# Optimization experiments

Measured on AMD Instinct MI355X. Metric: run time of the kernel, lower is better.

The kernel has to match this reference:

```python
import jax, jax.numpy as jnp
import numpy as np

K = 16
D = 1024
B = 65536

# Row-major off-diagonal index order matching the torch double loop (i, j, i != j)
_ii, _jj = np.nonzero(~np.eye(K, dtype=bool))  # each (K*(K-1),), row-major
OFF_I = jnp.asarray(_ii)
OFF_J = jnp.asarray(_jj)
DIAG = jnp.arange(K)


def setup_inputs() -> dict:
    key = jax.random.key(0)
    k1, k2, k3, k4, k5 = jax.random.split(key, 5)
    scale_d = 1.0 / np.sqrt(D)
    return {
        "x": jax.random.normal(k1, (B, D), dtype=jnp.float32),
        "Wd": jax.random.normal(k2, (K, D), dtype=jnp.float32) * scale_d,
        "bd": jax.random.normal(k3, (K,), dtype=jnp.float32) * 0.1,
        "Wo": jax.random.normal(k4, (K * (K - 1), D), dtype=jnp.float32) * scale_d,
        "bo": jax.random.normal(k5, (K * (K - 1),), dtype=jnp.float32) * 0.1 - 3.0,
    }


def reference(x, Wd, bd, Wo, bo):
    # Diagonal gates: (B, K)
    c_diag = jax.nn.sigmoid(jnp.einsum("bd,kd->bk", x, Wd) + bd)
    # Off-diagonal values: (B, K*(K-1)), non-positive
    off_vals = -jax.nn.softplus(jnp.einsum("bd,kd->bk", x, Wo) + bo)
    C = jnp.zeros((x.shape[0], K, K), dtype=x.dtype)
    C = C.at[:, OFF_I, OFF_J].set(off_vals)
    C = C.at[:, DIAG, DIAG].set(c_diag)
    return C
```

## Files before the change

### kernel.cpp

```cpp
#include <hip/hip_runtime.h>
#include <hip/hip_bf16.h>
#include <stdint.h>


typedef __bf16 bf16x8 __attribute__((ext_vector_type(8)));
typedef float f32x4 __attribute__((ext_vector_type(4)));

#define THREADS 512
#define BM 128
#define KSTEPS 16
#define WTILE 32768
#define WBYTES (WTILE * KSTEPS)

__device__ __forceinline__ unsigned bf_rtne(unsigned u) {
  return (u + 0x7fffu + ((u >> 16) & 1u)) >> 16;
}
__device__ __forceinline__ unsigned pack2(float lo, float hi) {
  return bf_rtne(__float_as_uint(lo)) | (bf_rtne(__float_as_uint(hi)) << 16);
}

__device__ __forceinline__ void gload_lds16(const void* g, void* l) {
  __builtin_amdgcn_global_load_lds(
      (const __attribute__((address_space(1))) unsigned int*)g,
      (__attribute__((address_space(3))) unsigned int*)l, 16, 0, 0);
}

__global__ void prep_kernel(const float* __restrict__ Wd, const float* __restrict__ bd,
                            const float* __restrict__ Wo, const float* __restrict__ bo,
                            char* __restrict__ wbuf, float* __restrict__ bias) {
  const int c = blockIdx.x;
  const int t = threadIdx.x;
  const int i = c >> 4, j = c & 15;
  const float* src;
  float b;
  if (i == j) { src = Wd + i * 1024; b = bd[i]; }
  else { int r = i * 15 + (j < i ? j : j - 1); src = Wo + r * 1024; b = bo[r]; }
  if (t == 0) bias[c] = b;
  const int kk = t * 4;
  const int kstep = kk >> 6, k6 = kk & 63;
  float4 v = *reinterpret_cast<const float4*>(src + kk);
  uint2 h;
  h.x = pack2(v.x, v.y);
  h.y = pack2(v.z, v.w);
  const unsigned off = (unsigned)((c * 128 + k6 * 2) ^ ((c & 7) << 4));
  *reinterpret_cast<uint2*>(wbuf + kstep * WTILE + off) = h;
}

__global__ __launch_bounds__(THREADS, 2) void cap_main(
    const float* __restrict__ x, const char* __restrict__ wbuf,
    const float* __restrict__ bias, float* __restrict__ out) {
  __shared__ char smem[98304];

  const int tid = threadIdx.x;
  const int wid = tid >> 6;
  const int lane = tid & 63;
  const int l15 = lane & 15;
  const int l4 = lane >> 4;
  const int wm = wid >> 2;
  const int wn = wid & 3;

  const size_t blkRow = (size_t)blockIdx.x * BM;

  const int f0 = tid * 8;
  const int f1 = f0 + 4096;
  const int ar0 = f0 >> 6, ac0 = f0 & 63;
  const int ar1 = f1 >> 6, ac1 = f1 & 63;
  const float* xs0 = x + (blkRow + (size_t)ar0) * 1024 + ac0;
  const float* xs1 = x + (blkRow + (size_t)ar1) * 1024 + ac1;
  const unsigned aw0 = (unsigned)((ar0 * 128 + ac0 * 2) ^ ((ar0 & 7) << 4));
  const unsigned aw1 = (unsigned)((ar1 * 128 + ac1 * 2) ^ ((ar1 & 7) << 4));

  const unsigned abase = (unsigned)((wm * 64 + l15) * 128 + l4 * 16);
  const unsigned bbase = (unsigned)((wn * 64 + l15) * 128 + l4 * 16);
  const unsigned sxor = (unsigned)((l15 & 7) << 4);

  f32x4 acc[4][4];
#pragma unroll
  for (int m = 0; m < 4; ++m)
#pragma unroll
    for (int n = 0; n < 4; ++n) acc[m][n] = (f32x4){0.f, 0.f, 0.f, 0.f};

  {
    float4 p0 = *reinterpret_cast<const float4*>(xs0);
    float4 p1 = *reinterpret_cast<const float4*>(xs0 + 4);
    float4 p2 = *reinterpret_cast<const float4*>(xs1);
    float4 p3 = *reinterpret_cast<const float4*>(xs1 + 4);
    char* Wn0 = smem + 32768;
#pragma unroll
    for (int r = 0; r < 4; ++r)
      gload_lds16(wbuf + r * 8192 + wid * 1024 + lane * 16, Wn0 + r * 8192 + wid * 1024);
    uint4 w0, w1;
    w0.x = pack2(p0.x, p0.y); w0.y = pack2(p0.z, p0.w);
    w0.z = pack2(p1.x, p1.y); w0.w = pack2(p1.z, p1.w);
    w1.x = pack2(p2.x, p2.y); w1.y = pack2(p2.z, p2.w);
    w1.z = pack2(p3.x, p3.y); w1.w = pack2(p3.z, p3.w);
    *reinterpret_cast<uint4*>(smem + aw0) = w0;
    *reinterpret_cast<uint4*>(smem + aw1) = w1;
  }
  __syncthreads();

  for (int t = 0; t < KSTEPS; ++t) {
    const int cur = t & 1;
    const char* Ac = smem + cur * 16384;
    const char* Bc = smem + 32768 + cur * 32768;
    char* An = smem + (cur ^ 1) * 16384;
    char* Wn = smem + 32768 + (cur ^ 1) * 32768;

    float4 n0, n1, n2, n3;
    if (t + 1 < KSTEPS) {
      const float* s0 = xs0 + (t + 1) * 64;
      const float* s1 = xs1 + (t + 1) * 64;
      n0 = *reinterpret_cast<const float4*>(s0);
      n1 = *reinterpret_cast<const float4*>(s0 + 4);
      n2 = *reinterpret_cast<const float4*>(s1);
      n3 = *reinterpret_cast<const float4*>(s1 + 4);
      const char* wsp = wbuf + (t + 1) * WTILE;
#pragma unroll
      for (int r = 0; r < 4; ++r)
        gload_lds16(wsp + r * 8192 + wid * 1024 + lane * 16, Wn + r * 8192 + wid * 1024);
    }

#pragma unroll
    for (int ks = 0; ks < 2; ++ks) {
      bf16x8 af[4], bfr[4];
#pragma unroll
      for (int m = 0; m < 4; ++m)
        af[m] = *reinterpret_cast<const bf16x8*>(Ac + ((abase + m * 2048 + ks * 64) ^ sxor));
#pragma unroll
      for (int n = 0; n < 4; ++n)
        bfr[n] = *reinterpret_cast<const bf16x8*>(Bc + ((bbase + n * 2048 + ks * 64) ^ sxor));
#pragma unroll
      for (int m = 0; m < 4; ++m)
#pragma unroll
        for (int n = 0; n < 4; ++n)
          acc[m][n] = __builtin_amdgcn_mfma_f32_16x16x32_bf16(af[m], bfr[n], acc[m][n], 0, 0, 0);
    }

    if (t + 1 < KSTEPS) {
      uint4 w0, w1;
      w0.x = pack2(n0.x, n0.y); w0.y = pack2(n0.z, n0.w);
      w0.z = pack2(n1.x, n1.y); w0.w = pack2(n1.z, n1.w);
      w1.x = pack2(n2.x, n2.y); w1.y = pack2(n2.z, n2.w);
      w1.z = pack2(n3.x, n3.y); w1.w = pack2(n3.z, n3.w);
      *reinterpret_cast<uint4*>(An + aw0) = w0;
      *reinterpret_cast<uint4*>(An + aw1) = w1;
    }
    __syncthreads();
  }

#pragma unroll
  for (int n = 0; n < 4; ++n) {
    const int col = wn * 64 + n * 16 + l15;
    const float bs = bias[col];
    const bool diag = (col % 17) == 0;
#pragma unroll
    for (int m = 0; m < 4; ++m) {
      const size_t row0 = blkRow + (size_t)(wm * 64 + m * 16 + l4 * 4);
#pragma unroll
      for (int j2 = 0; j2 < 4; ++j2) {
        float v = acc[m][n][j2] + bs;
        float e = __expf(-fabsf(v));
        float sig = (v >= 0.f) ? 1.f / (1.f + e) : e / (1.f + e);
        float sp = fmaxf(v, 0.f) + __logf(1.f + e);
        out[(row0 + j2) * 256 + col] = diag ? sig : -sp;
      }
    }
  }
}

extern "C" void kernel_launch(void* const* d_in, const int* in_sizes, int n_in,
                              void* d_out, int out_size, void* d_ws, size_t ws_size,
                              hipStream_t stream) {
  const float* x = (const float*)d_in[0];
  const float* Wd = (const float*)d_in[1];
  const float* bd = (const float*)d_in[2];
  const float* Wo = (const float*)d_in[3];
  const float* bo = (const float*)d_in[4];
  float* out = (float*)d_out;
  char* wbuf = (char*)d_ws;
  float* bias = (float*)(wbuf + WBYTES);

  prep_kernel<<<dim3(256), dim3(256), 0, stream>>>(Wd, bd, Wo, bo, wbuf, bias);
  cap_main<<<dim3(512), dim3(THREADS), 0, stream>>>(x, wbuf, bias, out);
}
```

Measured before the change: 107.8 us.

## Stream weight fragments from global directly, doubling threads and shrinking LDS

Prep now stores the bf16 weights in a fragment-ready layout so each lane can load its B operands straight from global/L2 into registers, which removes the weight tiles from shared memory. The block grows to 1024 threads (16 waves, each owning 32 rows by 64 columns), LDS drops to 32 KB for the A double buffer only, and the launch bound asks for 4 blocks per CU. The goal is higher occupancy and less LDS traffic for better latency hiding on this memory-bound GEMM. The cost is that every wave re-reads weights from cache each k-step with no prefetch ahead of the MFMAs, and the larger occupancy target limits registers per thread.

Result: slower. 124.4 us (+15.4%).

```diff
diff --git a/kernel.cpp b/kernel.cpp
--- a/kernel.cpp
+++ b/kernel.cpp
@@ -6,7 +6,7 @@
 typedef __bf16 bf16x8 __attribute__((ext_vector_type(8)));
 typedef float f32x4 __attribute__((ext_vector_type(4)));
 
-#define THREADS 512
+#define THREADS 1024
 #define BM 128
 #define KSTEPS 16
 #define WTILE 32768
@@ -17,12 +17,6 @@
 }
 __device__ __forceinline__ unsigned pack2(float lo, float hi) {
   return bf_rtne(__float_as_uint(lo)) | (bf_rtne(__float_as_uint(hi)) << 16);
-}
-
-__device__ __forceinline__ void gload_lds16(const void* g, void* l) {
-  __builtin_amdgcn_global_load_lds(
-      (const __attribute__((address_space(1))) unsigned int*)g,
-      (__attribute__((address_space(3))) unsigned int*)l, 16, 0, 0);
 }
 
 __global__ void prep_kernel(const float* __restrict__ Wd, const float* __restrict__ bd,
@@ -37,19 +31,18 @@
   else { int r = i * 15 + (j < i ? j : j - 1); src = Wo + r * 1024; b = bo[r]; }
   if (t == 0) bias[c] = b;
   const int kk = t * 4;
-  const int kstep = kk >> 6, k6 = kk & 63;
+  const int ts = kk >> 6, ks = (kk >> 5) & 1, q = (kk >> 3) & 3, e = kk & 7;
   float4 v = *reinterpret_cast<const float4*>(src + kk);
   uint2 h;
   h.x = pack2(v.x, v.y);
   h.y = pack2(v.z, v.w);
-  const unsigned off = (unsigned)((c * 128 + k6 * 2) ^ ((c & 7) << 4));
-  *reinterpret_cast<uint2*>(wbuf + kstep * WTILE + off) = h;
+  *reinterpret_cast<uint2*>(wbuf + ts * WTILE + ks * 16384 + q * 4096 + c * 16 + e * 2) = h;
 }
 
-__global__ __launch_bounds__(THREADS, 2) void cap_main(
+__global__ __launch_bounds__(THREADS, 4) void cap_main(
     const float* __restrict__ x, const char* __restrict__ wbuf,
     const float* __restrict__ bias, float* __restrict__ out) {
-  __shared__ char smem[98304];
+  __shared__ char smem[32768];
 
   const int tid = threadIdx.x;
   const int wid = tid >> 6;
@@ -61,89 +54,71 @@
 
   const size_t blkRow = (size_t)blockIdx.x * BM;
 
-  const int f0 = tid * 8;
-  const int f1 = f0 + 4096;
-  const int ar0 = f0 >> 6, ac0 = f0 & 63;
-  const int ar1 = f1 >> 6, ac1 = f1 & 63;
-  const float* xs0 = x + (blkRow + (size_t)ar0) * 1024 + ac0;
-  const float* xs1 = x + (blkRow + (size_t)ar1) * 1024 + ac1;
-  const unsigned aw0 = (unsigned)((ar0 * 128 + ac0 * 2) ^ ((ar0 & 7) << 4));
-  const unsigned aw1 = (unsigned)((ar1 * 128 + ac1 * 2) ^ ((ar1 & 7) << 4));
+  const int ar = tid >> 3;
+  const int ac = (tid & 7) * 8;
+  const float* xs = x + (blkRow + (size_t)ar) * 1024 + ac;
+  const unsigned aw = (unsigned)((ar * 128 + ac * 2) ^ ((ar & 7) << 4));
 
-  const unsigned abase = (unsigned)((wm * 64 + l15) * 128 + l4 * 16);
-  const unsigned bbase = (unsigned)((wn * 64 + l15) * 128 + l4 * 16);
+  const unsigned abase = (unsigned)((wm * 32 + l15) * 128 + l4 * 16);
   const unsigned sxor = (unsigned)((l15 & 7) << 4);
 
-  f32x4 acc[4][4];
+  const char* wb = wbuf + l4 * 4096 + (wn * 64 + l15) * 16;
+
+  f32x4 acc[2][4];
 #pragma unroll
-  for (int m = 0; m < 4; ++m)
+  for (int m = 0; m < 2; ++m)
 #pragma unroll
     for (int n = 0; n < 4; ++n) acc[m][n] = (f32x4){0.f, 0.f, 0.f, 0.f};
 
   {
-    float4 p0 = *reinterpret_cast<const float4*>(xs0);
-    float4 p1 = *reinterpret_cast<const float4*>(xs0 + 4);
-    float4 p2 = *reinterpret_cast<const float4*>(xs1);
-    float4 p3 = *reinterpret_cast<const float4*>(xs1 + 4);
-    char* Wn0 = smem + 32768;
-#pragma unroll
-    for (int r = 0; r < 4; ++r)
-      gload_lds16(wbuf + r * 8192 + wid * 1024 + lane * 16, Wn0 + r * 8192 + wid * 1024);
-    uint4 w0, w1;
-    w0.x = pack2(p0.x, p0.y); w0.y = pack2(p0.z, p0.w);
-    w0.z = pack2(p1.x, p1.y); w0.w = pack2(p1.z, p1.w);
-    w1.x = pack2(p2.x, p2.y); w1.y = pack2(p2.z, p2.w);
-    w1.z = pack2(p3.x, p3.y); w1.w = pack2(p3.z, p3.w);
-    *reinterpret_cast<uint4*>(smem + aw0) = w0;
-    *reinterpret_cast<uint4*>(smem + aw1) = w1;
+    float4 p0 = *reinterpret_cast<const float4*>(xs);
+    float4 p1 = *reinterpret_cast<const float4*>(xs + 4);
+    uint4 w;
+    w.x = pack2(p0.x, p0.y); w.y = pack2(p0.z, p0.w);
+    w.z = pack2(p1.x, p1.y); w.w = pack2(p1.z, p1.w);
+    *reinterpret_cast<uint4*>(smem + aw) = w;
   }
   __syncthreads();
 
   for (int t = 0; t < KSTEPS; ++t) {
     const int cur = t & 1;
     const char* Ac = smem + cur * 16384;
-    const char* Bc = smem + 32768 + cur * 32768;
     char* An = smem + (cur ^ 1) * 16384;
-    char* Wn = smem + 32768 + (cur ^ 1) * 32768;
 
-    float4 n0, n1, n2, n3;
+    float4 p0, p1;
     if (t + 1 < KSTEPS) {
-      const float* s0 = xs0 + (t + 1) * 64;
-      const float* s1 = xs1 + (t + 1) * 64;
-      n0 = *reinterpret_cast<const float4*>(s0);
-      n1 = *reinterpret_cast<const float4*>(s0 + 4);
-      n2 = *reinterpret_cast<const float4*>(s1);
-      n3 = *reinterpret_cast<const float4*>(s1 + 4);
-      const char* wsp = wbuf + (t + 1) * WTILE;
-#pragma unroll
-      for (int r = 0; r < 4; ++r)
-        gload_lds16(wsp + r * 8192 + wid * 1024 + lane * 16, Wn + r * 8192 + wid * 1024);
+      p0 = *reinterpret_cast<const float4*>(xs + (t + 1) * 64);
+      p1 = *reinterpret_cast<const float4*>(xs + (t + 1) * 64 + 4);
     }
 
+    const char* wt = wb + t * WTILE;
+    bf16x8 bfr[2][4];
 #pragma unroll
-    for (int ks = 0; ks < 2; ++ks) {
-      bf16x8 af[4], bfr[4];
-#pragma unroll
-      for (int m = 0; m < 4; ++m)
-        af[m] = *reinterpret_cast<const bf16x8*>(Ac + ((abase + m * 2048 + ks * 64) ^ sxor));
+    for (int ks = 0; ks < 2; ++ks)
 #pragma unroll
       for (int n = 0; n < 4; ++n)
-        bfr[n] = *reinterpret_cast<const bf16x8*>(Bc + ((bbase + n * 2048 + ks * 64) ^ sxor));
+        bfr[ks][n] = *reinterpret_cast<const bf16x8*>(wt + ks * 16384 + n * 256);
+
+    bf16x8 af[2][2];
 #pragma unroll
-      for (int m = 0; m < 4; ++m)
+    for (int ks = 0; ks < 2; ++ks)
+#pragma unroll
+      for (int m = 0; m < 2; ++m)
+        af[ks][m] = *reinterpret_cast<const bf16x8*>(Ac + ((abase + m * 2048 + ks * 64) ^ sxor));
+
+#pragma unroll
+    for (int ks = 0; ks < 2; ++ks)
+#pragma unroll
+      for (int m = 0; m < 2; ++m)
 #pragma unroll
         for (int n = 0; n < 4; ++n)
-          acc[m][n] = __builtin_amdgcn_mfma_f32_16x16x32_bf16(af[m], bfr[n], acc[m][n], 0, 0, 0);
-    }
+          acc[m][n] = __builtin_amdgcn_mfma_f32_16x16x32_bf16(af[ks][m], bfr[ks][n], acc[m][n], 0, 0, 0);
 
     if (t + 1 < KSTEPS) {
-      uint4 w0, w1;
-      w0.x = pack2(n0.x, n0.y); w0.y = pack2(n0.z, n0.w);
-      w0.z = pack2(n1.x, n1.y); w0.w = pack2(n1.z, n1.w);
-      w1.x = pack2(n2.x, n2.y); w1.y = pack2(n2.z, n2.w);
-      w1.z = pack2(n3.x, n3.y); w1.w = pack2(n3.z, n3.w);
-      *reinterpret_cast<uint4*>(An + aw0) = w0;
-      *reinterpret_cast<uint4*>(An + aw1) = w1;
+      uint4 w;
+      w.x = pack2(p0.x, p0.y); w.y = pack2(p0.z, p0.w);
+      w.z = pack2(p1.x, p1.y); w.w = pack2(p1.z, p1.w);
+      *reinterpret_cast<uint4*>(An + aw) = w;
     }
     __syncthreads();
   }
@@ -154,8 +129,8 @@
     const float bs = bias[col];
     const bool diag = (col % 17) == 0;
 #pragma unroll
-    for (int m = 0; m < 4; ++m) {
-      const size_t row0 = blkRow + (size_t)(wm * 64 + m * 16 + l4 * 4);
+    for (int m = 0; m < 2; ++m) {
+      const size_t row0 = blkRow + (size_t)(wm * 32 + m * 16 + l4 * 4);
 #pragma unroll
       for (int j2 = 0; j2 < 4; ++j2) {
         float v = acc[m][n][j2] + bs;
```

## Double the row tile to 256 per block and halve the grid

Applied to the files above, without the earlier changes.

Each block now covers 256 rows of x instead of 128, so every wave holds 8x4 accumulator tiles and the weight tile staged in LDS is reused across twice as many rows. The x loader is remapped so each thread fetches 8 float4s spaced 32 rows apart, and the grid drops from 512 to 256 blocks. This halves the total weight traffic into LDS. In exchange, register pressure and LDS use grow (128KB per block, which may allow only one block per CU), and 256 blocks on a 256-CU part leave less room for latency hiding.

New measurement: 107.9 us. About the same (+0.1%).

```diff
diff --git a/kernel.cpp b/kernel.cpp
--- a/kernel.cpp
+++ b/kernel.cpp
@@ -7,7 +7,7 @@
 typedef float f32x4 __attribute__((ext_vector_type(4)));
 
 #define THREADS 512
-#define BM 128
+#define BM 256
 #define KSTEPS 16
 #define WTILE 32768
 #define WBYTES (WTILE * KSTEPS)
@@ -49,7 +49,7 @@
 __global__ __launch_bounds__(THREADS, 2) void cap_main(
     const float* __restrict__ x, const char* __restrict__ wbuf,
     const float* __restrict__ bias, float* __restrict__ out) {
-  __shared__ char smem[98304];
+  __shared__ char smem[131072];
 
   const int tid = threadIdx.x;
   const int wid = tid >> 6;
@@ -61,89 +61,82 @@
 
   const size_t blkRow = (size_t)blockIdx.x * BM;
 
-  const int f0 = tid * 8;
-  const int f1 = f0 + 4096;
-  const int ar0 = f0 >> 6, ac0 = f0 & 63;
-  const int ar1 = f1 >> 6, ac1 = f1 & 63;
-  const float* xs0 = x + (blkRow + (size_t)ar0) * 1024 + ac0;
-  const float* xs1 = x + (blkRow + (size_t)ar1) * 1024 + ac1;
-  const unsigned aw0 = (unsigned)((ar0 * 128 + ac0 * 2) ^ ((ar0 & 7) << 4));
-  const unsigned aw1 = (unsigned)((ar1 * 128 + ac1 * 2) ^ ((ar1 & 7) << 4));
+  const int fr = tid >> 4;
+  const int fc = tid & 15;
+  const float* xs = x + (blkRow + (size_t)fr) * 1024 + fc * 4;
+  const unsigned aw0 = (unsigned)((fr * 128 + fc * 8) ^ ((fr & 7) << 4));
 
-  const unsigned abase = (unsigned)((wm * 64 + l15) * 128 + l4 * 16);
+  const unsigned abase = (unsigned)((wm * 128 + l15) * 128 + l4 * 16);
   const unsigned bbase = (unsigned)((wn * 64 + l15) * 128 + l4 * 16);
   const unsigned sxor = (unsigned)((l15 & 7) << 4);
 
-  f32x4 acc[4][4];
+  f32x4 acc[8][4];
 #pragma unroll
-  for (int m = 0; m < 4; ++m)
+  for (int m = 0; m < 8; ++m)
 #pragma unroll
     for (int n = 0; n < 4; ++n) acc[m][n] = (f32x4){0.f, 0.f, 0.f, 0.f};
 
   {
-    float4 p0 = *reinterpret_cast<const float4*>(xs0);
-    float4 p1 = *reinterpret_cast<const float4*>(xs0 + 4);
-    float4 p2 = *reinterpret_cast<const float4*>(xs1);
-    float4 p3 = *reinterpret_cast<const float4*>(xs1 + 4);
-    char* Wn0 = smem + 32768;
+    float4 xq[8];
+#pragma unroll
+    for (int q = 0; q < 8; ++q)
+      xq[q] = *reinterpret_cast<const float4*>(xs + q * 32 * 1024);
 #pragma unroll
     for (int r = 0; r < 4; ++r)
-      gload_lds16(wbuf + r * 8192 + wid * 1024 + lane * 16, Wn0 + r * 8192 + wid * 1024);
-    uint4 w0, w1;
-    w0.x = pack2(p0.x, p0.y); w0.y = pack2(p0.z, p0.w);
-    w0.z = pack2(p1.x, p1.y); w0.w = pack2(p1.z, p1.w);
-    w1.x = pack2(p2.x, p2.y); w1.y = pack2(p2.z, p2.w);
-    w1.z = pack2(p3.x, p3.y); w1.w = pack2(p3.z, p3.w);
-    *reinterpret_cast<uint4*>(smem + aw0) = w0;
-    *reinterpret_cast<uint4*>(smem + aw1) = w1;
+      gload_lds16(wbuf + r * 8192 + tid * 16, smem + 65536 + r * 8192 + wid * 1024);
+#pragma unroll
+    for (int q = 0; q < 8; ++q) {
+      uint2 h;
+      h.x = pack2(xq[q].x, xq[q].y);
+      h.y = pack2(xq[q].z, xq[q].w);
+      *reinterpret_cast<uint2*>(smem + aw0 + q * 4096) = h;
+    }
   }
   __syncthreads();
 
   for (int t = 0; t < KSTEPS; ++t) {
     const int cur = t & 1;
-    const char* Ac = smem + cur * 16384;
-    const char* Bc = smem + 32768 + cur * 32768;
-    char* An = smem + (cur ^ 1) * 16384;
-    char* Wn = smem + 32768 + (cur ^ 1) * 32768;
+    const char* Ac = smem + cur * 32768;
+    const char* Bc = smem + 65536 + cur * 32768;
+    char* An = smem + (cur ^ 1) * 32768;
+    char* Bn = smem + 65536 + (cur ^ 1) * 32768;
 
-    float4 n0, n1, n2, n3;
+    float4 xq[8];
     if (t + 1 < KSTEPS) {
-      const float* s0 = xs0 + (t + 1) * 64;
-      const float* s1 = xs1 + (t + 1) * 64;
-      n0 = *reinterpret_cast<const float4*>(s0);
-      n1 = *reinterpret_cast<const float4*>(s0 + 4);
-      n2 = *reinterpret_cast<const float4*>(s1);
-      n3 = *reinterpret_cast<const float4*>(s1 + 4);
+      const float* xsp = xs + (t + 1) * 64;
+#pragma unroll
+      for (int q = 0; q < 8; ++q)
+        xq[q] = *reinterpret_cast<const float4*>(xsp + q * 32 * 1024);
       const char* wsp = wbuf + (t + 1) * WTILE;
 #pragma unroll
       for (int r = 0; r < 4; ++r)
-        gload_lds16(wsp + r * 8192 + wid * 1024 + lane * 16, Wn + r * 8192 + wid * 1024);
+        gload_lds16(wsp + r * 8192 + tid * 16, Bn + r * 8192 + wid * 1024);
     }
 
 #pragma unroll
     for (int ks = 0; ks < 2; ++ks) {
-      bf16x8 af[4], bfr[4];
-#pragma unroll
-      for (int m = 0; m < 4; ++m)
-        af[m] = *reinterpret_cast<const bf16x8*>(Ac + ((abase + m * 2048 + ks * 64) ^ sxor));
+      bf16x8 bfr[4], af[8];
 #pragma unroll
       for (int n = 0; n < 4; ++n)
         bfr[n] = *reinterpret_cast<const bf16x8*>(Bc + ((bbase + n * 2048 + ks * 64) ^ sxor));
 #pragma unroll
-      for (int m = 0; m < 4; ++m)
+      for (int m = 0; m < 8; ++m)
+        af[m] = *reinterpret_cast<const bf16x8*>(Ac + ((abase + m * 2048 + ks * 64) ^ sxor));
+#pragma unroll
+      for (int m = 0; m < 8; ++m)
 #pragma unroll
         for (int n = 0; n < 4; ++n)
           acc[m][n] = __builtin_amdgcn_mfma_f32_16x16x32_bf16(af[m], bfr[n], acc[m][n], 0, 0, 0);
     }
 
     if (t + 1 < KSTEPS) {
-      uint4 w0, w1;
-      w0.x = pack2(n0.x, n0.y); w0.y = pack2(n0.z, n0.w);
-      w0.z = pack2(n1.x, n1.y); w0.w = pack2(n1.z, n1.w);
-      w1.x = pack2(n2.x, n2.y); w1.y = pack2(n2.z, n2.w);
-      w1.z = pack2(n3.x, n3.y); w1.w = pack2(n3.z, n3.w);
-      *reinterpret_cast<uint4*>(An + aw0) = w0;
-      *reinterpret_cast<uint4*>(An + aw1) = w1;
+#pragma unroll
+      for (int q = 0; q < 8; ++q) {
+        uint2 h;
+        h.x = pack2(xq[q].x, xq[q].y);
+        h.y = pack2(xq[q].z, xq[q].w);
+        *reinterpret_cast<uint2*>(An + aw0 + q * 4096) = h;
+      }
     }
     __syncthreads();
   }
@@ -154,8 +147,8 @@
     const float bs = bias[col];
     const bool diag = (col % 17) == 0;
 #pragma unroll
-    for (int m = 0; m < 4; ++m) {
-      const size_t row0 = blkRow + (size_t)(wm * 64 + m * 16 + l4 * 4);
+    for (int m = 0; m < 8; ++m) {
+      const size_t row0 = blkRow + (size_t)(wm * 128 + m * 16 + l4 * 4);
 #pragma unroll
       for (int j2 = 0; j2 < 4; ++j2) {
         float v = acc[m][n][j2] + bs;
@@ -181,5 +174,5 @@
   float* bias = (float*)(wbuf + WBYTES);
 
   prep_kernel<<<dim3(256), dim3(256), 0, stream>>>(Wd, bd, Wo, bo, wbuf, bias);
-  cap_main<<<dim3(512), dim3(THREADS), 0, stream>>>(x, wbuf, bias, out);
+  cap_main<<<dim3(256), dim3(THREADS), 0, stream>>>(x, wbuf, bias, out);
 }
```
